# Performance work log

Measured on AMD Instinct MI355X. Metric: run time of the kernel, lower is better.

The kernel has to match this reference:

```python
import jax, jax.numpy as jnp
import numpy as np

EPS = 1e-6
NEG_SLOPE = 0.2
LN_EPS = 1e-6


def _evn_nonlinearity(x, wa, ba, wb, bb):
    # x: (..., F, D); norm over the vector axis F (axis=-2)
    norm = jnp.linalg.norm(x, axis=-2, keepdims=True)  # (..., 1, D)
    zero_norm = norm <= EPS
    norm = norm + EPS
    h = jax.nn.leaky_relu(norm @ wa + ba, NEG_SLOPE)   # (..., 1, D//2)
    g = h @ wb + bb                                    # (..., 1, D)
    # skip_connection == 0: rescale direction by learned norm gate
    return jnp.where(zero_norm, x, x / norm * g)


def _layernorm(x, scale, bias):
    mean = jnp.mean(x, axis=-1, keepdims=True)
    var = jnp.var(x, axis=-1, keepdims=True)
    return (x - mean) * jax.lax.rsqrt(var + LN_EPS) * scale + bias


def setup_inputs() -> dict:
    key = jax.random.key(0)
    ks = jax.random.split(key, 12)
    B, N, F, D = 8, 2048, 3, 256
    QK, V, H, Q = 512, 512, 8, 64
    dh, dv = QK // H, V // H
    s = lambda *sh: 1.0 / np.sqrt(sh[0])
    return {
        "x": jax.random.normal(ks[0], (B, N, F, D), jnp.float32),
        "lq": jax.random.normal(ks[1], (Q, QK), jnp.float32) * s(QK),
        "w_kv": jax.random.normal(ks[2], (D, QK), jnp.float32) * s(D),
        "w_evn1a": jax.random.normal(ks[3], (QK, QK // 2), jnp.float32) * s(QK),
        "b_evn1a": jnp.zeros((QK // 2,), jnp.float32),
        "w_evn1b": jax.random.normal(ks[4], (QK // 2, QK), jnp.float32) * s(QK // 2),
        "b_evn1b": jnp.zeros((QK,), jnp.float32),
        "wq": jax.random.normal(ks[5], (QK, H, dh), jnp.float32) * s(QK),
        "wk": jax.random.normal(ks[6], (QK, H, dh), jnp.float32) * s(QK),
        "wv": jax.random.normal(ks[7], (QK, H, dv), jnp.float32) * s(QK),
        "ln_q_scale": jnp.ones((dh,), jnp.float32),
        "ln_q_bias": jnp.zeros((dh,), jnp.float32),
        "ln_k_scale": jnp.ones((dh,), jnp.float32),
        "ln_k_bias": jnp.zeros((dh,), jnp.float32),
        "w_out": jax.random.normal(ks[8], (V, V), jnp.float32) * s(V),
        "w_evn2a": jax.random.normal(ks[9], (V, V // 2), jnp.float32) * s(V),
        "b_evn2a": jnp.zeros((V // 2,), jnp.float32),
        "w_evn2b": jax.random.normal(ks[10], (V // 2, V), jnp.float32) * s(V // 2),
        "b_evn2b": jnp.zeros((V,), jnp.float32),
    }


def reference(x, lq, w_kv, w_evn1a, b_evn1a, w_evn1b, b_evn1b, wq, wk, wv,
              ln_q_scale, ln_q_bias, ln_k_scale, ln_k_bias,
              w_out, w_evn2a, b_evn2a, w_evn2b, b_evn2b):
    B, N, F, _ = x.shape
    H = wq.shape[1]
    # EVLinearLeakyReLU: Dense (no bias) + EVN nonlinearity
    kv = _evn_nonlinearity(x @ w_kv, w_evn1a, b_evn1a, w_evn1b, b_evn1b)  # (B,N,F,QK)
    # invariant features: contract vector axis with its channel-mean
    kv_inv = jnp.einsum('bnfd,bnf->bnd', kv, jnp.mean(kv, axis=-1))       # (B,N,QK)
    q = jnp.einsum('qd,dhe->hqe', lq, wq)          # (H,Q,dh)
    k = jnp.einsum('bnd,dhe->hbne', kv_inv, wk)    # (H,B,N,dh)
    v = jnp.einsum('bnfd,dhe->hbnfe', kv, wv)      # (H,B,N,F,dv)
    # normalize_qk
    q = _layernorm(q, ln_q_scale, ln_q_bias)
    k = _layernorm(k, ln_k_scale, ln_k_bias)
    scale = np.sqrt(k.shape[-1]).astype(np.float32)
    attn = jnp.einsum('hqi,hbki->hbqk', q, k)      # (H,B,Q,N)
    attn = jax.nn.softmax(attn / scale, axis=-1)
    resi = jnp.einsum('hbqk,hbkfd->hbqfd', attn, v)  # (H,B,Q,F,dv)
    # 'h b q f d -> b q f (h d)'
    resi = jnp.moveaxis(resi, 0, -2)
    resi = resi.reshape(*resi.shape[:-2], -1)        # (B,Q,F,V)
    resi = _evn_nonlinearity(resi @ w_out, w_evn2a, b_evn2a, w_evn2b, b_evn2b)
    return resi
```

## Files before the change

### kernel.cpp

```cpp
#include <hip/hip_runtime.h>
#include <hip/hip_bf16.h>

typedef _Float16 f16;
typedef __attribute__((ext_vector_type(8))) _Float16 f16x8;
typedef __attribute__((ext_vector_type(4))) _Float16 f16x4;
typedef __attribute__((ext_vector_type(2))) _Float16 f16x2;
typedef __attribute__((ext_vector_type(4))) float floatx4;

constexpr int B  = 8;
constexpr int N  = 2048;
constexpr int Fv = 3;
constexpr int Dd = 256;
constexpr int QK = 512;
constexpr int Vd = 512;
constexpr int Hh = 8;
constexpr int Qq = 64;
constexpr int DH = 64;
constexpr int NT = B * N;
constexpr float EPS = 1e-6f;
constexpr float NEG = 0.2f;
constexpr float LNE = 1e-6f;

#define DEV static __device__ __forceinline__
DEV void split(float v, f16& h, f16& l) { h = (f16)v; l = (f16)(v - (float)h); }

template<int ASRC, int EPI>
__global__ __launch_bounds__(256) void k_gemm3(
    const float* __restrict__ A32,
    const f16* __restrict__ Ah, const f16* __restrict__ Al,
    const f16* __restrict__ Bh, const f16* __restrict__ Bl,
    int Ndim, int Kdim, void* __restrict__ C1, void* __restrict__ C2,
    const float* __restrict__ e0, const float* __restrict__ e1)
{
    __shared__ __align__(16) f16 Ash[128][72];
    __shared__ __align__(16) f16 Asl[128][72];
    __shared__ __align__(16) f16 Bsh[64][72];
    __shared__ __align__(16) f16 Bsl[64][72];

    const int t = threadIdx.x;
    long row0; int col0, boff;
    if (EPI == 5) { row0 = (long)blockIdx.y * 1536 + (long)blockIdx.x * 128; col0 = 0; boff = blockIdx.y * 64; }
    else          { row0 = (long)blockIdx.x * 128; col0 = blockIdx.y * 64; boff = 0; }

    floatx4 acc0[4], acc1[4];
    #pragma unroll
    for (int nt = 0; nt < 4; ++nt)
        #pragma unroll
        for (int j = 0; j < 4; ++j) { acc0[nt][j] = 0.f; acc1[nt][j] = 0.f; }

    const int L = t & 63, w = t >> 6;
    const int kq = (L >> 4) << 3;

    for (int k0 = 0; k0 < Kdim; k0 += 64) {
        if constexpr (ASRC == 1) {
            #pragma unroll
            for (int j = 0; j < 8; ++j) {
                const int i = t + j * 256;
                const int r = i >> 4, c4 = (i & 15) << 2;
                const floatx4 v = *(const floatx4*)&A32[(row0 + r) * Kdim + k0 + c4];
                f16x4 h4, l4;
                #pragma unroll
                for (int m = 0; m < 4; ++m) { h4[m] = (f16)v[m]; l4[m] = (f16)(v[m] - (float)h4[m]); }
                *(f16x4*)&Ash[r][c4] = h4;
                *(f16x4*)&Asl[r][c4] = l4;
            }
        } else {
            #pragma unroll
            for (int j = 0; j < 4; ++j) {
                const int i = t + j * 256;
                const int r = i >> 3, c8 = (i & 7) << 3;
                *(f16x8*)&Ash[r][c8] = *(const f16x8*)&Ah[(row0 + r) * (long)Kdim + k0 + c8];
                *(f16x8*)&Asl[r][c8] = *(const f16x8*)&Al[(row0 + r) * (long)Kdim + k0 + c8];
            }
        }
        #pragma unroll
        for (int j = 0; j < 2; ++j) {
            const int i = t + j * 256;
            const int r = i >> 3, c8 = (i & 7) << 3;
            *(f16x8*)&Bsh[r][c8] = *(const f16x8*)&Bh[(long)(boff + col0 + r) * Kdim + k0 + c8];
            *(f16x8*)&Bsl[r][c8] = *(const f16x8*)&Bl[(long)(boff + col0 + r) * Kdim + k0 + c8];
        }
        __syncthreads();
        #pragma unroll
        for (int kk = 0; kk < 64; kk += 32) {
            const f16x8 ah0 = *(const f16x8*)&Ash[w * 32 + (L & 15)][kk + kq];
            const f16x8 al0 = *(const f16x8*)&Asl[w * 32 + (L & 15)][kk + kq];
            const f16x8 ah1 = *(const f16x8*)&Ash[w * 32 + 16 + (L & 15)][kk + kq];
            const f16x8 al1 = *(const f16x8*)&Asl[w * 32 + 16 + (L & 15)][kk + kq];
            #pragma unroll
            for (int nt = 0; nt < 4; ++nt) {
                const f16x8 bh = *(const f16x8*)&Bsh[nt * 16 + (L & 15)][kk + kq];
                const f16x8 bl = *(const f16x8*)&Bsl[nt * 16 + (L & 15)][kk + kq];
                acc0[nt] = __builtin_amdgcn_mfma_f32_16x16x32_f16(ah0, bh, acc0[nt], 0, 0, 0);
                acc0[nt] = __builtin_amdgcn_mfma_f32_16x16x32_f16(ah0, bl, acc0[nt], 0, 0, 0);
                acc0[nt] = __builtin_amdgcn_mfma_f32_16x16x32_f16(al0, bh, acc0[nt], 0, 0, 0);
                acc1[nt] = __builtin_amdgcn_mfma_f32_16x16x32_f16(ah1, bh, acc1[nt], 0, 0, 0);
                acc1[nt] = __builtin_amdgcn_mfma_f32_16x16x32_f16(ah1, bl, acc1[nt], 0, 0, 0);
                acc1[nt] = __builtin_amdgcn_mfma_f32_16x16x32_f16(al1, bh, acc1[nt], 0, 0, 0);
            }
        }
        __syncthreads();
    }

    const int cb = L & 15;
    #pragma unroll
    for (int rt = 0; rt < 2; ++rt) {
        const floatx4* acc = rt ? acc1 : acc0;
        const int rb = w * 32 + rt * 16 + ((L >> 4) << 2);
        if constexpr (EPI == 0) {
            f16* Ch = (f16*)C1; f16* Cl = (f16*)C2;
            #pragma unroll
            for (int nt = 0; nt < 4; ++nt)
                #pragma unroll
                for (int r = 0; r < 4; ++r) {
                    f16 h, l; split(acc[nt][r], h, l);
                    const long o = (row0 + rb + r) * (long)Ndim + col0 + nt * 16 + cb;
                    Ch[o] = h; Cl[o] = l;
                }
        } else if constexpr (EPI == 1) {
            f16* Ch = (f16*)C1; f16* Cl = (f16*)C2;
            #pragma unroll
            for (int nt = 0; nt < 4; ++nt) {
                const int col = col0 + nt * 16 + cb;
                const float bias = e0[col];
                #pragma unroll
                for (int r = 0; r < 4; ++r) {
                    float v = acc[nt][r] + bias;
                    v = v > 0.f ? v : NEG * v;
                    f16 h, l; split(v, h, l);
                    const long o = (row0 + rb + r) * (long)Ndim + col;
                    Ch[o] = h; Cl[o] = l;
                }
            }
        } else if constexpr (EPI == 2) {
            float* C = (float*)C1;
            #pragma unroll
            for (int nt = 0; nt < 4; ++nt) {
                const int col = col0 + nt * 16 + cb;
                const float bias = e0[col];
                #pragma unroll
                for (int r = 0; r < 4; ++r)
                    C[(row0 + rb + r) * (long)Ndim + col] = acc[nt][r] + bias;
            }
        } else if constexpr (EPI == 3) {
            f16* Ch = (f16*)C1; f16* Cl = (f16*)C2;
            const int h = blockIdx.y;
            #pragma unroll
            for (int r = 0; r < 4; ++r) {
                float s = 0.f, q = 0.f;
                #pragma unroll
                for (int nt = 0; nt < 4; ++nt) { const float v = acc[nt][r]; s += v; q += v * v; }
                s += __shfl_xor(s, 1); q += __shfl_xor(q, 1);
                s += __shfl_xor(s, 2); q += __shfl_xor(q, 2);
                s += __shfl_xor(s, 4); q += __shfl_xor(q, 4);
                s += __shfl_xor(s, 8); q += __shfl_xor(q, 8);
                const float mean = s * (1.f / 64.f);
                const float var  = q * (1.f / 64.f) - mean * mean;
                const float rs   = rsqrtf(var + LNE);
                #pragma unroll
                for (int nt = 0; nt < 4; ++nt) {
                    const int col = nt * 16 + cb;
                    const float v = (acc[nt][r] - mean) * rs * e0[col] + e1[col];
                    f16 hh, ll; split(v, hh, ll);
                    const long o = ((long)h * NT + row0 + rb + r) * 64 + col;
                    Ch[o] = hh; Cl[o] = ll;
                }
            }
        } else {
            float* C = (float*)C1;
            #pragma unroll
            for (int nt = 0; nt < 4; ++nt)
                #pragma unroll
                for (int r = 0; r < 4; ++r) {
                    const long rr = row0 + rb + r - (long)blockIdx.y * 1536;
                    C[rr * 512 + boff + nt * 16 + cb] = acc[nt][r];
                }
        }
    }
}

__global__ __launch_bounds__(256) void k_attn_mfma(
    const f16* __restrict__ qh, const f16* __restrict__ ql,
    const f16* __restrict__ kh, const f16* __restrict__ kl,
    f16* __restrict__ ath, f16* __restrict__ atl, float* __restrict__ lsum_part)
{
    __shared__ __align__(16) f16 Qh[64][72], Ql[64][72];
    __shared__ __align__(16) f16 Kh[64][72], Kl[64][72];

    const int t = threadIdx.x;
    const int bx = blockIdx.x;
    const int hb = bx & 63;
    const int part = bx >> 6;
    const int h = hb >> 3;
    const int L = t & 63, w = t >> 6;
    const int kq = (L >> 4) << 3;

    #pragma unroll
    for (int j = 0; j < 2; ++j) {
        const int i = t + j * 256;
        const int r = i >> 3, c8 = (i & 7) << 3;
        *(f16x8*)&Qh[r][c8] = *(const f16x8*)&qh[((long)h * 64 + r) * 64 + c8];
        *(f16x8*)&Ql[r][c8] = *(const f16x8*)&ql[((long)h * 64 + r) * 64 + c8];
    }
    __syncthreads();

    f16x8 qah[2], qal[2];
    #pragma unroll
    for (int kc = 0; kc < 2; ++kc) {
        qah[kc] = *(const f16x8*)&Qh[w * 16 + (L & 15)][kc * 32 + kq];
        qal[kc] = *(const f16x8*)&Ql[w * 16 + (L & 15)][kc * 32 + kq];
    }

    float psum[4] = {0.f, 0.f, 0.f, 0.f};
    const int rowb = w * 16 + ((L >> 4) << 2);

    for (int nt0 = 0; nt0 < 4; ++nt0) {
        const int n0 = part * 256 + nt0 * 64;
        __syncthreads();
        #pragma unroll
        for (int j = 0; j < 2; ++j) {
            const int i = t + j * 256;
            const int r = i >> 3, c8 = (i & 7) << 3;
            *(f16x8*)&Kh[r][c8] = *(const f16x8*)&kh[((long)hb * N + n0 + r) * 64 + c8];
            *(f16x8*)&Kl[r][c8] = *(const f16x8*)&kl[((long)hb * N + n0 + r) * 64 + c8];
        }
        __syncthreads();

        floatx4 acc[4];
        #pragma unroll
        for (int nt = 0; nt < 4; ++nt)
            #pragma unroll
            for (int j = 0; j < 4; ++j) acc[nt][j] = 0.f;

        #pragma unroll
        for (int kc = 0; kc < 2; ++kc) {
            #pragma unroll
            for (int nt = 0; nt < 4; ++nt) {
                const f16x8 bh = *(const f16x8*)&Kh[nt * 16 + (L & 15)][kc * 32 + kq];
                const f16x8 bl = *(const f16x8*)&Kl[nt * 16 + (L & 15)][kc * 32 + kq];
                acc[nt] = __builtin_amdgcn_mfma_f32_16x16x32_f16(qah[kc], bh, acc[nt], 0, 0, 0);
                acc[nt] = __builtin_amdgcn_mfma_f32_16x16x32_f16(qah[kc], bl, acc[nt], 0, 0, 0);
                acc[nt] = __builtin_amdgcn_mfma_f32_16x16x32_f16(qal[kc], bh, acc[nt], 0, 0, 0);
            }
        }

        #pragma unroll
        for (int nt = 0; nt < 4; ++nt)
            #pragma unroll
            for (int r = 0; r < 4; ++r) {
                const float p = __expf(acc[nt][r] * 0.125f);
                psum[r] += p;
                f16 hh, ll; split(p, hh, ll);
                const long o = ((long)hb * 64 + rowb + r) * N + n0 + nt * 16 + (L & 15);
                ath[o] = hh; atl[o] = ll;
            }
    }

    #pragma unroll
    for (int r = 0; r < 4; ++r) {
        float s = psum[r];
        s += __shfl_xor(s, 1);
        s += __shfl_xor(s, 2);
        s += __shfl_xor(s, 4);
        s += __shfl_xor(s, 8);
        if ((L & 15) == 0) lsum_part[part * 4096 + hb * 64 + rowb + r] = s;
    }
}

__global__ void k_lsum_reduce(const float* __restrict__ part, float* __restrict__ lsum)
{
    const int i = blockIdx.x * 256 + threadIdx.x;
    float s = 0.f;
    #pragma unroll
    for (int p = 0; p < 8; ++p) s += part[p * 4096 + i];
    lsum[i] = s;
}

__global__ __launch_bounds__(512, 4) void k_gemm3T(
    const f16* __restrict__ Ah, const f16* __restrict__ Al,
    const f16* __restrict__ Bh, const f16* __restrict__ Bl,
    const float* __restrict__ lsum,
    f16* __restrict__ Uh, f16* __restrict__ Ul)
{
    __shared__ __align__(16) f16 Ash[128][72];
    __shared__ __align__(16) f16 Asl[128][72];
    __shared__ __align__(16) f16 Bsh[96][72];
    __shared__ __align__(16) f16 Bsl[96][72];

    const int t = threadIdx.x;
    const int by = blockIdx.x;
    const int b = by & 7;
    const int rest = by >> 3;
    const int ct = rest & 15;
    const int hp = rest >> 4;
    const int hb0 = b + 16 * hp;
    const int hb1 = hb0 + 8;
    const f16* A0h = Ah + (long)hb0 * 64 * 2048;
    const f16* A0l = Al + (long)hb0 * 64 * 2048;
    const f16* A1h = Ah + (long)hb1 * 64 * 2048;
    const f16* A1l = Al + (long)hb1 * 64 * 2048;
    const f16* Bbh = Bh + (long)b * 2048 * 1536 + ct * 96;
    const f16* Bbl = Bl + (long)b * 2048 * 1536 + ct * 96;

    floatx4 acc[2][3];
    #pragma unroll
    for (int i = 0; i < 2; ++i)
        #pragma unroll
        for (int nt = 0; nt < 3; ++nt)
            #pragma unroll
            for (int j = 0; j < 4; ++j) acc[i][nt][j] = 0.f;

    const int L = t & 63, w = t >> 6;
    const int wr = (w >> 1) << 5;
    const int wc = (w & 1) * 48;
    const int kq = (L >> 4) << 3;
    const int ar = t >> 3, ac = (t & 7) << 3;
    const int k2 = t & 31, c8 = (t >> 5) << 3;
    const bool bstage = t < 384;

    f16x8 pA0h, pA1h, pA0l, pA1l;
    f16x8 pB0h, pB1h, pB0l, pB1l;
    {
        pA0h = *(const f16x8*)&A0h[(long)ar * 2048 + ac];
        pA1h = *(const f16x8*)&A1h[(long)ar * 2048 + ac];
        pA0l = *(const f16x8*)&A0l[(long)ar * 2048 + ac];
        pA1l = *(const f16x8*)&A1l[(long)ar * 2048 + ac];
        if (bstage) {
            pB0h = *(const f16x8*)&Bbh[(long)(2 * k2) * 1536 + c8];
            pB1h = *(const f16x8*)&Bbh[(long)(2 * k2 + 1) * 1536 + c8];
            pB0l = *(const f16x8*)&Bbl[(long)(2 * k2) * 1536 + c8];
            pB1l = *(const f16x8*)&Bbl[(long)(2 * k2 + 1) * 1536 + c8];
        }
    }

    for (int k0 = 0; k0 < 2048; k0 += 64) {
        *(f16x8*)&Ash[ar][ac]      = pA0h;
        *(f16x8*)&Ash[ar + 64][ac] = pA1h;
        *(f16x8*)&Asl[ar][ac]      = pA0l;
        *(f16x8*)&Asl[ar + 64][ac] = pA1l;
        if (bstage) {
            #pragma unroll
            for (int j = 0; j < 8; ++j) {
                f16x2 ph; ph[0] = pB0h[j]; ph[1] = pB1h[j];
                f16x2 pl; pl[0] = pB0l[j]; pl[1] = pB1l[j];
                *(f16x2*)&Bsh[c8 + j][2 * k2] = ph;
                *(f16x2*)&Bsl[c8 + j][2 * k2] = pl;
            }
        }
        __syncthreads();

        if (k0 + 64 < 2048) {
            const int kn = k0 + 64;
            pA0h = *(const f16x8*)&A0h[(long)ar * 2048 + kn + ac];
            pA1h = *(const f16x8*)&A1h[(long)ar * 2048 + kn + ac];
            pA0l = *(const f16x8*)&A0l[(long)ar * 2048 + kn + ac];
            pA1l = *(const f16x8*)&A1l[(long)ar * 2048 + kn + ac];
            if (bstage) {
                pB0h = *(const f16x8*)&Bbh[(long)(kn + 2 * k2) * 1536 + c8];
                pB1h = *(const f16x8*)&Bbh[(long)(kn + 2 * k2 + 1) * 1536 + c8];
                pB0l = *(const f16x8*)&Bbl[(long)(kn + 2 * k2) * 1536 + c8];
                pB1l = *(const f16x8*)&Bbl[(long)(kn + 2 * k2 + 1) * 1536 + c8];
            }
        }

        #pragma unroll
        for (int kk = 0; kk < 64; kk += 32) {
            const f16x8 ah0 = *(const f16x8*)&Ash[wr + (L & 15)][kk + kq];
            const f16x8 al0 = *(const f16x8*)&Asl[wr + (L & 15)][kk + kq];
            const f16x8 ah1 = *(const f16x8*)&Ash[wr + 16 + (L & 15)][kk + kq];
            const f16x8 al1 = *(const f16x8*)&Asl[wr + 16 + (L & 15)][kk + kq];
            #pragma unroll
            for (int nt = 0; nt < 3; ++nt) {
                const f16x8 bh = *(const f16x8*)&Bsh[wc + nt * 16 + (L & 15)][kk + kq];
                const f16x8 bl = *(const f16x8*)&Bsl[wc + nt * 16 + (L & 15)][kk + kq];
                acc[0][nt] = __builtin_amdgcn_mfma_f32_16x16x32_f16(ah0, bh, acc[0][nt], 0, 0, 0);
                acc[0][nt] = __builtin_amdgcn_mfma_f32_16x16x32_f16(ah0, bl, acc[0][nt], 0, 0, 0);
                acc[0][nt] = __builtin_amdgcn_mfma_f32_16x16x32_f16(al0, bh, acc[0][nt], 0, 0, 0);
                acc[1][nt] = __builtin_amdgcn_mfma_f32_16x16x32_f16(ah1, bh, acc[1][nt], 0, 0, 0);
                acc[1][nt] = __builtin_amdgcn_mfma_f32_16x16x32_f16(ah1, bl, acc[1][nt], 0, 0, 0);
                acc[1][nt] = __builtin_amdgcn_mfma_f32_16x16x32_f16(al1, bh, acc[1][nt], 0, 0, 0);
            }
        }
        __syncthreads();
    }

    const int cb = L & 15;
    #pragma unroll
    for (int rt = 0; rt < 2; ++rt) {
        const int rloc = wr + rt * 16 + ((L >> 4) << 2);
        const int hb = (rloc < 64) ? hb0 : hb1;
        #pragma unroll
        for (int r = 0; r < 4; ++r) {
            const int q = (rloc + r) & 63;
            const float inv = 1.f / lsum[hb * 64 + q];
            #pragma unroll
            for (int nt = 0; nt < 3; ++nt) {
                f16 h, l; split(acc[rt][nt][r] * inv, h, l);
                const long o = ((long)hb * 64 + q) * 1536 + ct * 96 + wc + nt * 16 + cb;
                Uh[o] = h; Ul[o] = l;
            }
        }
    }
}

__global__ void k_castTpair(const float* __restrict__ s, f16* __restrict__ dh,
                            f16* __restrict__ dl, int K, int Nn)
{
    const long i = (long)blockIdx.x * 256 + threadIdx.x;
    if (i >= (long)K * Nn) return;
    const int k = (int)(i / Nn), n = (int)(i - (long)k * Nn);
    f16 h, l; split(s[i], h, l);
    dh[(long)n * K + k] = h;
    dl[(long)n * K + k] = l;
}

__global__ void k_norm(const f16* __restrict__ kh, const f16* __restrict__ kl,
                       f16* __restrict__ nh, f16* __restrict__ nl)
{
    const long i = (long)blockIdx.x * 256 + threadIdx.x;
    const int tk = (int)(i >> 9), c = (int)(i & 511);
    const long base = (long)tk * 1536 + c;
    const float a = (float)kh[base]        + (float)kl[base];
    const float b = (float)kh[base + 512]  + (float)kl[base + 512];
    const float cc = (float)kh[base + 1024] + (float)kl[base + 1024];
    f16 h, l; split(sqrtf(a * a + b * b + cc * cc) + EPS, h, l);
    nh[i] = h; nl[i] = l;
}

__global__ __launch_bounds__(256) void k_gate(
    f16* __restrict__ kh, f16* __restrict__ kl, const float* __restrict__ g,
    f16* __restrict__ kih, f16* __restrict__ kil)
{
    __shared__ float red[3][4];
    const int t = threadIdx.x;
    const int tk = blockIdx.x;
    float kv[2][3];
    float ps0 = 0.f, ps1 = 0.f, ps2 = 0.f;
    #pragma unroll
    for (int j = 0; j < 2; ++j) {
        const int c = t + j * 256;
        const long base = (long)tk * 1536 + c;
        const float k0 = (float)kh[base]        + (float)kl[base];
        const float k1 = (float)kh[base + 512]  + (float)kl[base + 512];
        const float k2 = (float)kh[base + 1024] + (float)kl[base + 1024];
        const float nr = sqrtf(k0 * k0 + k1 * k1 + k2 * k2);
        const float gv = g[(long)tk * 512 + c];
        const float s = (nr <= EPS) ? 1.f : gv / (nr + EPS);
        kv[j][0] = k0 * s; kv[j][1] = k1 * s; kv[j][2] = k2 * s;
        f16 h, l;
        split(kv[j][0], h, l); kh[base] = h;        kl[base] = l;
        split(kv[j][1], h, l); kh[base + 512] = h;  kl[base + 512] = l;
        split(kv[j][2], h, l); kh[base + 1024] = h; kl[base + 1024] = l;
        ps0 += kv[j][0]; ps1 += kv[j][1]; ps2 += kv[j][2];
    }
    for (int off = 32; off; off >>= 1) {
        ps0 += __shfl_down(ps0, off);
        ps1 += __shfl_down(ps1, off);
        ps2 += __shfl_down(ps2, off);
    }
    if ((t & 63) == 0) { red[0][t >> 6] = ps0; red[1][t >> 6] = ps1; red[2][t >> 6] = ps2; }
    __syncthreads();
    const float m0 = (red[0][0] + red[0][1] + red[0][2] + red[0][3]) * (1.f / 512.f);
    const float m1 = (red[1][0] + red[1][1] + red[1][2] + red[1][3]) * (1.f / 512.f);
    const float m2 = (red[2][0] + red[2][1] + red[2][2] + red[2][3]) * (1.f / 512.f);
    #pragma unroll
    for (int j = 0; j < 2; ++j) {
        const int c = t + j * 256;
        f16 h, l; split(kv[j][0] * m0 + kv[j][1] * m1 + kv[j][2] * m2, h, l);
        kih[(long)tk * 512 + c] = h;
        kil[(long)tk * 512 + c] = l;
    }
}

__global__ __launch_bounds__(256) void k_gate2(
    const f16* __restrict__ rph, const f16* __restrict__ rpl,
    const float* __restrict__ g2, float* __restrict__ out)
{
    const int t = threadIdx.x;
    const int tk = blockIdx.x;
    #pragma unroll
    for (int j = 0; j < 2; ++j) {
        const int c = t + j * 256;
        const long base = (long)tk * 1536 + c;
        const float r0 = (float)rph[base]        + (float)rpl[base];
        const float r1 = (float)rph[base + 512]  + (float)rpl[base + 512];
        const float r2 = (float)rph[base + 1024] + (float)rpl[base + 1024];
        const float nr = sqrtf(r0 * r0 + r1 * r1 + r2 * r2);
        const float gv = g2[(long)tk * 512 + c];
        const float s = (nr <= EPS) ? 1.f : gv / (nr + EPS);
        out[base]        = r0 * s;
        out[base + 512]  = r1 * s;
        out[base + 1024] = r2 * s;
    }
}

__global__ __launch_bounds__(256) void k_qproj(
    const float* __restrict__ lq, const float* __restrict__ wq,
    const float* __restrict__ lns, const float* __restrict__ lnb,
    f16* __restrict__ qh, f16* __restrict__ ql)
{
    __shared__ float cs[QK];
    const int t = threadIdx.x;
    const int qi = blockIdx.x;
    const float* cp = lq + (long)qi * QK;
    for (int i = t; i < QK; i += 256) cs[i] = cp[i];
    __syncthreads();

    float a0 = 0, a1 = 0;
    #pragma unroll 4
    for (int d = 0; d < QK; ++d) {
        const float c = cs[d];
        a0 += c * wq[d * QK + t];
        a1 += c * wq[d * QK + t + 256];
    }
    float s0 = a0, q0 = a0 * a0, s1 = a1, q1 = a1 * a1;
    for (int off = 32; off; off >>= 1) {
        s0 += __shfl_down(s0, off); q0 += __shfl_down(q0, off);
        s1 += __shfl_down(s1, off); q1 += __shfl_down(q1, off);
    }
    s0 = __shfl(s0, 0); q0 = __shfl(q0, 0);
    s1 = __shfl(s1, 0); q1 = __shfl(q1, 0);
    const float mean0 = s0 * (1.f / 64.f), var0 = q0 * (1.f / 64.f) - mean0 * mean0;
    const float mean1 = s1 * (1.f / 64.f), var1 = q1 * (1.f / 64.f) - mean1 * mean1;
    const int e = t & 63;
    const float sc = lns[e], bi = lnb[e];
    const float r0 = (a0 - mean0) * rsqrtf(var0 + LNE) * sc + bi;
    const float r1 = (a1 - mean1) * rsqrtf(var1 + LNE) * sc + bi;
    const int h0 = t >> 6, h1 = h0 + 4;
    f16 h, l;
    split(r0, h, l);
    qh[((long)h0 * Qq + qi) * DH + e] = h;
    ql[((long)h0 * Qq + qi) * DH + e] = l;
    split(r1, h, l);
    qh[((long)h1 * Qq + qi) * DH + e] = h;
    ql[((long)h1 * Qq + qi) * DH + e] = l;
}

extern "C" void kernel_launch(void* const* d_in, const int* in_sizes, int n_in,
                              void* d_out, int out_size, void* d_ws, size_t ws_size,
                              hipStream_t stream)
{
    const float* x    = (const float*)d_in[0];
    const float* lq   = (const float*)d_in[1];
    const float* w_kv = (const float*)d_in[2];
    const float* w1a  = (const float*)d_in[3];
    const float* b1a  = (const float*)d_in[4];
    const float* w1b  = (const float*)d_in[5];
    const float* b1b  = (const float*)d_in[6];
    const float* wq   = (const float*)d_in[7];
    const float* wk   = (const float*)d_in[8];
    const float* wv   = (const float*)d_in[9];
    const float* lqs  = (const float*)d_in[10];
    const float* lqb  = (const float*)d_in[11];
    const float* lks  = (const float*)d_in[12];
    const float* lkb  = (const float*)d_in[13];
    const float* wo   = (const float*)d_in[14];
    const float* w2a  = (const float*)d_in[15];
    const float* b2a  = (const float*)d_in[16];
    const float* w2b  = (const float*)d_in[17];
    const float* b2b  = (const float*)d_in[18];

    char* ws = (char*)d_ws;
    f16* wkvTh = (f16*)(ws + 0);
    f16* wkvTl = (f16*)(ws + 262144);
    f16* w1aTh = (f16*)(ws + 524288);
    f16* w1aTl = (f16*)(ws + 786432);
    f16* w1bTh = (f16*)(ws + 1048576);
    f16* w1bTl = (f16*)(ws + 1310720);
    f16* wkTh  = (f16*)(ws + 1572864);
    f16* wkTl  = (f16*)(ws + 2097152);
    f16* wvTh  = (f16*)(ws + 2621440);
    f16* wvTl  = (f16*)(ws + 3145728);
    f16*   qhp   = (f16*)(ws + 3670016);
    f16*   qlp   = (f16*)(ws + 3735552);
    float* lsum  = (float*)(ws + 3801088);
    f16* woTh  = (f16*)(ws + 3817472);
    f16* woTl  = (f16*)(ws + 4341760);
    f16* w2aTh = (f16*)(ws + 4866048);
    f16* w2aTl = (f16*)(ws + 5128192);
    f16* w2bTh = (f16*)(ws + 5390336);
    f16* w2bTl = (f16*)(ws + 5652480);
    float* lsum_part = (float*)(ws + 5914624);
    f16* nh    = (f16*)(ws + 6946816);
    f16* nl    = (f16*)(ws + 23724032);
    f16* kih   = nh;
    f16* kil   = nl;
    f16* ath   = (f16*)(ws + 6946816);
    f16* atl   = (f16*)(ws + 23724032);
    f16*   rph  = (f16*)(ws + 6946816);
    f16*   rpl  = (f16*)(ws + 8519680);
    f16*   n2h  = (f16*)(ws + 10092544);
    f16*   n2l  = (f16*)(ws + 10616832);
    f16*   h2h  = (f16*)(ws + 11141120);
    f16*   h2l  = (f16*)(ws + 11403264);
    float* g2   = (float*)(ws + 11665408);
    f16* hbh   = (f16*)(ws + 40501248);
    f16* hbl   = (f16*)(ws + 48889856);
    float* resiT = (float*)(ws + 40501248);
    f16* kvh   = (f16*)(ws + 57278464);
    f16* kvl   = (f16*)(ws + 107610112);
    float* g    = (float*)(ws + 157941760);
    f16* khb   = (f16*)(ws + 157941760);
    f16* klb   = (f16*)(ws + 174718976);
    f16* Uh    = (f16*)(ws + 157941760);
    f16* Ul    = (f16*)(ws + 170524672);
    float* out  = (float*)d_out;

    k_castTpair<<<512,  256, 0, stream>>>(w_kv, wkvTh, wkvTl, Dd, QK);
    k_castTpair<<<512,  256, 0, stream>>>(w1a,  w1aTh, w1aTl, QK, 256);
    k_castTpair<<<512,  256, 0, stream>>>(w1b,  w1bTh, w1bTl, 256, QK);
    k_castTpair<<<1024, 256, 0, stream>>>(wk,   wkTh,  wkTl,  QK, QK);
    k_castTpair<<<1024, 256, 0, stream>>>(wv,   wvTh,  wvTl,  QK, QK);
    k_castTpair<<<1024, 256, 0, stream>>>(wo,   woTh,  woTl,  Vd, Vd);
    k_castTpair<<<512,  256, 0, stream>>>(w2a,  w2aTh, w2aTl, Vd, 256);
    k_castTpair<<<512,  256, 0, stream>>>(w2b,  w2bTh, w2bTl, 256, Vd);

    k_gemm3<1, 0><<<dim3(384, 8), 256, 0, stream>>>(
        x, nullptr, nullptr, wkvTh, wkvTl, QK, Dd, kvh, kvl, nullptr, nullptr);
    k_norm<<<32768, 256, 0, stream>>>(kvh, kvl, nh, nl);
    k_gemm3<0, 1><<<dim3(128, 4), 256, 0, stream>>>(
        nullptr, nh, nl, w1aTh, w1aTl, 256, QK, hbh, hbl, b1a, nullptr);
    k_gemm3<0, 2><<<dim3(128, 8), 256, 0, stream>>>(
        nullptr, hbh, hbl, w1bTh, w1bTl, QK, 256, g, nullptr, b1b, nullptr);
    k_gate<<<NT, 256, 0, stream>>>(kvh, kvl, g, kih, kil);
    k_gemm3<0, 3><<<dim3(128, 8), 256, 0, stream>>>(
        nullptr, kih, kil, wkTh, wkTl, QK, QK, khb, klb, lks, lkb);
    k_qproj<<<Qq, 256, 0, stream>>>(lq, wq, lqs, lqb, qhp, qlp);
    k_attn_mfma<<<512, 256, 0, stream>>>(qhp, qlp, khb, klb, ath, atl, lsum_part);
    k_lsum_reduce<<<16, 256, 0, stream>>>(lsum_part, lsum);
    k_gemm3T<<<512, 512, 0, stream>>>(ath, atl, kvh, kvl, lsum, Uh, Ul);
    k_gemm3<0, 5><<<dim3(12, 8), 256, 0, stream>>>(
        nullptr, Uh, Ul, wvTh, wvTl, 64, QK, resiT, nullptr, nullptr, nullptr);
    k_gemm3<1, 0><<<dim3(12, 8), 256, 0, stream>>>(
        resiT, nullptr, nullptr, woTh, woTl, Vd, Vd, rph, rpl, nullptr, nullptr);
    k_norm<<<1024, 256, 0, stream>>>(rph, rpl, n2h, n2l);
    k_gemm3<0, 1><<<dim3(4, 4), 256, 0, stream>>>(
        nullptr, n2h, n2l, w2aTh, w2aTl, 256, Vd, h2h, h2l, b2a, nullptr);
    k_gemm3<0, 2><<<dim3(4, 8), 256, 0, stream>>>(
        nullptr, h2h, h2l, w2bTh, w2bTl, Vd, 256, g2, nullptr, b2b, nullptr);
    k_gate2<<<B * Qq, 256, 0, stream>>>(rph, rpl, g2, out);
}
```

Measured before the change: 586.0 us.

## Double-buffer LDS in gemm3T with K-step 32 and one sync per iteration

Restructures the k_gemm3T main loop so the shared-memory tiles are double-buffered and the K step drops from 64 to 32. Each iteration now loads the next global tile, computes on the current buffer and writes the other buffer, with a single barrier per step instead of two. This cuts barrier count per K element and lets global loads overlap MFMA work. The trade-offs are twice as many loop iterations, unpadded 32-wide LDS rows that may cause bank conflicts, and fewer threads staging B.

```diff
diff --git a/kernel.cpp b/kernel.cpp
--- a/kernel.cpp
+++ b/kernel.cpp
@@ -282,10 +282,10 @@
     const float* __restrict__ lsum,
     f16* __restrict__ Uh, f16* __restrict__ Ul)
 {
-    __shared__ __align__(16) f16 Ash[128][72];
-    __shared__ __align__(16) f16 Asl[128][72];
-    __shared__ __align__(16) f16 Bsh[96][72];
-    __shared__ __align__(16) f16 Bsl[96][72];
+    __shared__ __align__(16) f16 Ash[2][128][32];
+    __shared__ __align__(16) f16 Asl[2][128][32];
+    __shared__ __align__(16) f16 Bsh[2][96][32];
+    __shared__ __align__(16) f16 Bsl[2][96][32];
 
     const int t = threadIdx.x;
     const int by = blockIdx.x;
@@ -295,12 +295,21 @@
     const int hp = rest >> 4;
     const int hb0 = b + 16 * hp;
     const int hb1 = hb0 + 8;
-    const f16* A0h = Ah + (long)hb0 * 64 * 2048;
-    const f16* A0l = Al + (long)hb0 * 64 * 2048;
-    const f16* A1h = Ah + (long)hb1 * 64 * 2048;
-    const f16* A1l = Al + (long)hb1 * 64 * 2048;
+
+    const int ar = t >> 2;
+    const int aseg = (t & 3) << 3;
+    const f16* Arh = (ar < 64)
+        ? Ah + ((long)hb0 * 64 + ar) * 2048
+        : Ah + ((long)hb1 * 64 + (ar - 64)) * 2048;
+    const f16* Arl = (ar < 64)
+        ? Al + ((long)hb0 * 64 + ar) * 2048
+        : Al + ((long)hb1 * 64 + (ar - 64)) * 2048;
+
     const f16* Bbh = Bh + (long)b * 2048 * 1536 + ct * 96;
     const f16* Bbl = Bl + (long)b * 2048 * 1536 + ct * 96;
+    const bool bstage = t < 192;
+    const int k2 = t & 15;
+    const int cg = t >> 4;
 
     floatx4 acc[2][3];
     #pragma unroll
@@ -314,73 +323,61 @@
     const int wr = (w >> 1) << 5;
     const int wc = (w & 1) * 48;
     const int kq = (L >> 4) << 3;
-    const int ar = t >> 3, ac = (t & 7) << 3;
-    const int k2 = t & 31, c8 = (t >> 5) << 3;
-    const bool bstage = t < 384;
-
-    f16x8 pA0h, pA1h, pA0l, pA1l;
-    f16x8 pB0h, pB1h, pB0l, pB1l;
-    {
-        pA0h = *(const f16x8*)&A0h[(long)ar * 2048 + ac];
-        pA1h = *(const f16x8*)&A1h[(long)ar * 2048 + ac];
-        pA0l = *(const f16x8*)&A0l[(long)ar * 2048 + ac];
-        pA1l = *(const f16x8*)&A1l[(long)ar * 2048 + ac];
+
+    f16x8 pAh, pAl, pB0h, pB1h, pB0l, pB1l;
+
+    auto LOAD = [&](int k0) {
+        pAh = *(const f16x8*)&Arh[k0 + aseg];
+        pAl = *(const f16x8*)&Arl[k0 + aseg];
         if (bstage) {
-            pB0h = *(const f16x8*)&Bbh[(long)(2 * k2) * 1536 + c8];
-            pB1h = *(const f16x8*)&Bbh[(long)(2 * k2 + 1) * 1536 + c8];
-            pB0l = *(const f16x8*)&Bbl[(long)(2 * k2) * 1536 + c8];
-            pB1l = *(const f16x8*)&Bbl[(long)(2 * k2 + 1) * 1536 + c8];
-        }
-    }
-
-    for (int k0 = 0; k0 < 2048; k0 += 64) {
-        *(f16x8*)&Ash[ar][ac]      = pA0h;
-        *(f16x8*)&Ash[ar + 64][ac] = pA1h;
-        *(f16x8*)&Asl[ar][ac]      = pA0l;
-        *(f16x8*)&Asl[ar + 64][ac] = pA1l;
+            const long r0 = (long)(k0 + 2 * k2) * 1536 + cg * 8;
+            pB0h = *(const f16x8*)&Bbh[r0];
+            pB1h = *(const f16x8*)&Bbh[r0 + 1536];
+            pB0l = *(const f16x8*)&Bbl[r0];
+            pB1l = *(const f16x8*)&Bbl[r0 + 1536];
+        }
+    };
+    auto WRITE = [&](int buf) {
+        *(f16x8*)&Ash[buf][ar][aseg] = pAh;
+        *(f16x8*)&Asl[buf][ar][aseg] = pAl;
         if (bstage) {
             #pragma unroll
             for (int j = 0; j < 8; ++j) {
                 f16x2 ph; ph[0] = pB0h[j]; ph[1] = pB1h[j];
                 f16x2 pl; pl[0] = pB0l[j]; pl[1] = pB1l[j];
-                *(f16x2*)&Bsh[c8 + j][2 * k2] = ph;
-                *(f16x2*)&Bsl[c8 + j][2 * k2] = pl;
-            }
-        }
-        __syncthreads();
-
-        if (k0 + 64 < 2048) {
-            const int kn = k0 + 64;
-            pA0h = *(const f16x8*)&A0h[(long)ar * 2048 + kn + ac];
-            pA1h = *(const f16x8*)&A1h[(long)ar * 2048 + kn + ac];
-            pA0l = *(const f16x8*)&A0l[(long)ar * 2048 + kn + ac];
-            pA1l = *(const f16x8*)&A1l[(long)ar * 2048 + kn + ac];
-            if (bstage) {
-                pB0h = *(const f16x8*)&Bbh[(long)(kn + 2 * k2) * 1536 + c8];
-                pB1h = *(const f16x8*)&Bbh[(long)(kn + 2 * k2 + 1) * 1536 + c8];
-                pB0l = *(const f16x8*)&Bbl[(long)(kn + 2 * k2) * 1536 + c8];
-                pB1l = *(const f16x8*)&Bbl[(long)(kn + 2 * k2 + 1) * 1536 + c8];
-            }
-        }
-
-        #pragma unroll
-        for (int kk = 0; kk < 64; kk += 32) {
-            const f16x8 ah0 = *(const f16x8*)&Ash[wr + (L & 15)][kk + kq];
-            const f16x8 al0 = *(const f16x8*)&Asl[wr + (L & 15)][kk + kq];
-            const f16x8 ah1 = *(const f16x8*)&Ash[wr + 16 + (L & 15)][kk + kq];
-            const f16x8 al1 = *(const f16x8*)&Asl[wr + 16 + (L & 15)][kk + kq];
-            #pragma unroll
-            for (int nt = 0; nt < 3; ++nt) {
-                const f16x8 bh = *(const f16x8*)&Bsh[wc + nt * 16 + (L & 15)][kk + kq];
-                const f16x8 bl = *(const f16x8*)&Bsl[wc + nt * 16 + (L & 15)][kk + kq];
-                acc[0][nt] = __builtin_amdgcn_mfma_f32_16x16x32_f16(ah0, bh, acc[0][nt], 0, 0, 0);
-                acc[0][nt] = __builtin_amdgcn_mfma_f32_16x16x32_f16(ah0, bl, acc[0][nt], 0, 0, 0);
-                acc[0][nt] = __builtin_amdgcn_mfma_f32_16x16x32_f16(al0, bh, acc[0][nt], 0, 0, 0);
-                acc[1][nt] = __builtin_amdgcn_mfma_f32_16x16x32_f16(ah1, bh, acc[1][nt], 0, 0, 0);
-                acc[1][nt] = __builtin_amdgcn_mfma_f32_16x16x32_f16(ah1, bl, acc[1][nt], 0, 0, 0);
-                acc[1][nt] = __builtin_amdgcn_mfma_f32_16x16x32_f16(al1, bh, acc[1][nt], 0, 0, 0);
-            }
-        }
+                *(f16x2*)&Bsh[buf][cg * 8 + j][2 * k2] = ph;
+                *(f16x2*)&Bsl[buf][cg * 8 + j][2 * k2] = pl;
+            }
+        }
+    };
+    auto COMPUTE = [&](int buf) {
+        const f16x8 ah0 = *(const f16x8*)&Ash[buf][wr + (L & 15)][kq];
+        const f16x8 al0 = *(const f16x8*)&Asl[buf][wr + (L & 15)][kq];
+        const f16x8 ah1 = *(const f16x8*)&Ash[buf][wr + 16 + (L & 15)][kq];
+        const f16x8 al1 = *(const f16x8*)&Asl[buf][wr + 16 + (L & 15)][kq];
+        #pragma unroll
+        for (int nt = 0; nt < 3; ++nt) {
+            const f16x8 bh = *(const f16x8*)&Bsh[buf][wc + nt * 16 + (L & 15)][kq];
+            const f16x8 bl = *(const f16x8*)&Bsl[buf][wc + nt * 16 + (L & 15)][kq];
+            acc[0][nt] = __builtin_amdgcn_mfma_f32_16x16x32_f16(ah0, bh, acc[0][nt], 0, 0, 0);
+            acc[0][nt] = __builtin_amdgcn_mfma_f32_16x16x32_f16(ah0, bl, acc[0][nt], 0, 0, 0);
+            acc[0][nt] = __builtin_amdgcn_mfma_f32_16x16x32_f16(al0, bh, acc[0][nt], 0, 0, 0);
+            acc[1][nt] = __builtin_amdgcn_mfma_f32_16x16x32_f16(ah1, bh, acc[1][nt], 0, 0, 0);
+            acc[1][nt] = __builtin_amdgcn_mfma_f32_16x16x32_f16(ah1, bl, acc[1][nt], 0, 0, 0);
+            acc[1][nt] = __builtin_amdgcn_mfma_f32_16x16x32_f16(al1, bh, acc[1][nt], 0, 0, 0);
+        }
+    };
+
+    LOAD(0);
+    WRITE(0);
+    __syncthreads();
+
+    #pragma unroll 2
+    for (int tt = 0; tt < 64; ++tt) {
+        const int cur = tt & 1;
+        if (tt < 63) LOAD((tt + 1) * 32);
+        COMPUTE(cur);
+        if (tt < 63) WRITE(cur ^ 1);
         __syncthreads();
     }
 
```

Measured after the change: 579.7 us. Within noise of the previous version (-1.1%).
